# Performance work log

Measured on AMD Instinct MI355X. Metric: run time of the kernel, lower is better.

Reference implementation:

```python
import jax, jax.numpy as jnp
import numpy as np

# ---------- e3nn-style machinery, max_l = 1, real basis ----------
_EPS3 = np.zeros((3, 3, 3), dtype=np.float64)
_EPS3[0, 1, 2] = _EPS3[1, 2, 0] = _EPS3[2, 0, 1] = 1.0
_EPS3[0, 2, 1] = _EPS3[2, 1, 0] = _EPS3[1, 0, 2] = -1.0
W3J = {
    (0, 0, 0): np.ones((1, 1, 1)),
    (0, 1, 1): np.eye(3)[None, :, :] / np.sqrt(3.0),
    (1, 0, 1): np.eye(3)[:, None, :] / np.sqrt(3.0),
    (1, 1, 0): np.eye(3)[:, :, None] / np.sqrt(3.0),
    (1, 1, 1): _EPS3 / np.sqrt(6.0),
}

# irreps as (mul, l, parity)
IR_SH    = [(1, 0, 1), (1, 1, -1)]                      # 1x0e+1x1o (dim 4)
IR_INTER = [(4, 0, 1), (4, 0, -1), (2, 1, -1), (2, 1, 1)]  # gate.irreps_in (dim 20)
IR_GOUT  = [(2, 0, 1), (2, 0, -1), (2, 1, -1), (2, 1, 1)]  # gate.irreps_out (dim 16)
IR_OUT   = [(1, 1, -1), (1, 1, 1)]                      # 1x1o+1x1e (dim 6)

def _offsets(ir):
    off, o = [], 0
    for m, l, _ in ir:
        off.append(o)
        o += m * (2 * l + 1)
    return off, o

def build_tp(ir1, ir2, iro):
    """Fully-connected TP instructions: component irrep-norm, element path-norm."""
    fan = [0.0] * len(iro)
    paths = []
    for io, (mo, lo, po) in enumerate(iro):
        for i1, (m1, l1, p1) in enumerate(ir1):
            for i2, (m2, l2, p2) in enumerate(ir2):
                if p1 * p2 == po and abs(l1 - l2) <= lo <= l1 + l2:
                    paths.append((i1, i2, io))
                    fan[io] += m1 * m2
    ins, woff = [], 0
    for i1, i2, io in paths:
        m1, l1, _ = ir1[i1]; m2, l2, _ = ir2[i2]; mo, lo, _ = iro[io]
        alpha = float(np.sqrt((2 * lo + 1) / fan[io]))
        ins.append((i1, i2, io, alpha, woff))
        woff += m1 * m2 * mo
    return ins, woff

INS1, NUMEL1 = build_tp(IR_SH, IR_SH, IR_INTER)   # weight_numel = 14
INS2, NUMEL2 = build_tp(IR_GOUT, IR_SH, IR_OUT)   # weight_numel = 12

def tp_apply(ir1, ir2, iro, ins, x1, x2, w):
    off1, _ = _offsets(ir1); off2, _ = _offsets(ir2); offo, _ = _offsets(iro)
    lead = x1.shape[:-1]
    out = [None] * len(iro)
    for i1, i2, io, alpha, woff in ins:
        m1, l1, _ = ir1[i1]; m2, l2, _ = ir2[i2]; mo, lo, _ = iro[io]
        x1b = x1[..., off1[i1]:off1[i1] + m1 * (2 * l1 + 1)].reshape(lead + (m1, 2 * l1 + 1))
        x2b = x2[..., off2[i2]:off2[i2] + m2 * (2 * l2 + 1)].reshape(lead + (m2, 2 * l2 + 1))
        wb = w[..., woff:woff + m1 * m2 * mo].reshape(lead + (m1, m2, mo))
        C = jnp.asarray(W3J[(l1, l2, lo)], dtype=x1.dtype)
        blk = alpha * jnp.einsum('...ui,...vj,ijk,...uvw->...wk', x1b, x2b, C, wb)
        out[io] = blk if out[io] is None else out[io] + blk
    pieces = []
    for io, (mo, lo, _) in enumerate(iro):
        b = out[io] if out[io] is not None else jnp.zeros(lead + (mo, 2 * lo + 1), x1.dtype)
        pieces.append(b.reshape(lead + (mo * (2 * lo + 1),)))
    return jnp.concatenate(pieces, axis=-1)

def fc_net(x, w1, w2):
    # e3nn FullyConnectedNet: h = relu(x @ W1 / sqrt(fan_in)) * sqrt(2); out = h @ W2 / sqrt(fan)
    h = jax.nn.relu(x @ w1 / np.sqrt(w1.shape[0])) * np.sqrt(2.0)
    return h @ w2 / np.sqrt(w2.shape[0])

def gate_fn(x):
    # input irreps: [4x0e | 4x0o | 2x1o | 2x1e]; within 0e: 2 scalars + gates g1,g3; within 0o: 2 scalars + gates g2,g4
    lead = x.shape[:-1]
    se = jax.nn.relu(x[..., 0:2])
    ge = x[..., 2:4]
    so = jnp.abs(x[..., 4:6])
    go = x[..., 6:8]
    v1o = x[..., 8:14].reshape(lead + (2, 3))
    v1e = x[..., 14:20].reshape(lead + (2, 3))
    g1 = jax.nn.relu(ge[..., 0:1]); g3 = jax.nn.relu(ge[..., 1:2])
    g2 = jnp.tanh(go[..., 0:1]);    g4 = jnp.tanh(go[..., 1:2])
    v1o_out = jnp.concatenate([v1o[..., 0, :] * g1, v1o[..., 1, :] * g2], axis=-1)
    v1e_out = jnp.concatenate([v1e[..., 0, :] * g3, v1e[..., 1, :] * g4], axis=-1)
    return jnp.concatenate([se, so, v1o_out, v1e_out], axis=-1)  # [..., 16]

def sph_l1(d):
    # spherical harmonics l<=1, normalize=True, normalization='component' (e3nn l=1 order: y,z,x)
    n = jnp.sqrt(jnp.sum(d * d, axis=-1, keepdims=True) + 1e-12)
    u = d / n
    ones = jnp.ones(d.shape[:-1] + (1,), d.dtype)
    return jnp.concatenate([ones, np.sqrt(3.0) * u[..., [1, 2, 0]]], axis=-1)  # [..., 4]

def global_conv(ir1, iro, ins, nf, edge_attr, atten, normalizer, w1, w2):
    w = fc_net(atten, w1, w2)                                   # [B,N,N,numel]
    B, N = nf.shape[0], nf.shape[1]
    nfe = jnp.broadcast_to(nf[:, None, :, :], (B, N, N, nf.shape[-1]))  # node j at edge (i,j)
    ef = tp_apply(ir1, IR_SH, iro, ins, nfe, edge_attr, w)      # [B,N,N,dim_out]
    return jnp.sum(ef, axis=1) / normalizer

def _forward(attn_disp, attn_mask, coordinates, fc1_w1, fc1_w2, fc2_w1, fc2_w2):
    B, H, N, _ = attn_disp.shape
    normalizer = jnp.sqrt(jnp.sum((~jnp.isinf(attn_disp[:, 0])).astype(coordinates.dtype), axis=-1))[..., None]  # [B,N,1]
    ad = jnp.transpose(attn_disp, (0, 2, 3, 1))                 # [B,N,N,H]
    ad = jnp.where(jnp.isinf(ad), jnp.zeros((), ad.dtype), ad)
    # unit displacement (zero on diagonal)
    d = coordinates[:, :, None, :] - coordinates[:, None, :, :]
    d = d / (jnp.sqrt(jnp.sum(d * d, axis=-1, keepdims=True) + 1e-12) + 1e-5)
    edge_features = sph_l1(d)                                   # [B,N,N,4]
    nf = jnp.sum(edge_features, axis=1) / normalizer            # [B,N,4]
    nf = global_conv(IR_SH, IR_INTER, INS1, nf, edge_features, ad, normalizer, fc1_w1, fc1_w2)   # [B,N,20]
    nf = gate_fn(nf)                                            # [B,N,16]
    nf = global_conv(IR_GOUT, IR_OUT, INS2, nf, edge_features, ad, normalizer, fc2_w1, fc2_w2)   # [B,N,6]
    return ad, attn_mask, coordinates, nf, edge_features

def setup_inputs() -> dict:
    key = jax.random.key(0)
    ks = jax.random.split(key, 8)
    B, H, N = 4, 16, 512
    return {
        'attn_disp': jax.random.normal(ks[0], (B, H, N, N), jnp.float32),
        'attn_mask': jax.random.normal(ks[1], (B * H, N, N), jnp.float32),
        'coordinates': jax.random.normal(ks[2], (B, N, 3), jnp.float32),
        'fc1_w1': jax.random.normal(ks[3], (H, 2 * H), jnp.float32),
        'fc1_w2': jax.random.normal(ks[4], (2 * H, NUMEL1), jnp.float32),
        'fc2_w1': jax.random.normal(ks[5], (H, 2 * H), jnp.float32),
        'fc2_w2': jax.random.normal(ks[6], (2 * H, NUMEL2), jnp.float32),
    }

def reference(attn_disp, attn_mask, coordinates, fc1_w1, fc1_w2, fc2_w1, fc2_w2):
    return _forward(attn_disp, attn_mask, coordinates, fc1_w1, fc1_w2, fc2_w1, fc2_w2)
```

## Files before the change

kernel.cpp:

```cpp
#include <hip/hip_runtime.h>
#include <cmath>

#define NN 512

__device__ __forceinline__ int is_inf_f(float x) {
    return (__float_as_uint(x) & 0x7fffffffu) == 0x7f800000u;
}

__device__ __forceinline__ void edge_vec(float ci0, float ci1, float ci2,
                                         float cj0, float cj1, float cj2,
                                         float& e0, float& e1, float& e2) {
    float d0 = ci0 - cj0, d1 = ci1 - cj1, d2 = ci2 - cj2;
    float den = sqrtf(d0*d0 + d1*d1 + d2*d2 + 1e-12f) + 1e-5f;
    float r = 1.0f / den;
    d0 *= r; d1 *= r; d2 *= r;
    float n = sqrtf(d0*d0 + d1*d1 + d2*d2 + 1e-12f);
    float s = 1.7320508075688772f / n;
    e0 = d1 * s;
    e1 = d2 * s;
    e2 = d0 * s;
}

__global__ __launch_bounds__(256) void k_trans(
    const float* __restrict__ disp, const float* __restrict__ coords,
    float* __restrict__ ad_out, float* __restrict__ adT_out,
    float* __restrict__ ef_out, float* __restrict__ ws_norm)
{
    __shared__ float L[256 * 20];
    const int blk = blockIdx.x;
    const int b   = blk >> 7;
    const int i0  = (blk & 127) << 2;
    const int tid = threadIdx.x;
    const int il  = tid >> 6;
    const int jl  = tid & 63;
    const int i   = i0 + il;
    const float ci0 = coords[(b*NN+i)*3+0];
    const float ci1 = coords[(b*NN+i)*3+1];
    const float ci2 = coords[(b*NN+i)*3+2];
    int cnt = 0;
    for (int ch = 0; ch < 8; ch++) {
        const int j = ch*64 + jl;
        float v[16];
        #pragma unroll
        for (int h = 0; h < 16; h++) {
            float x = disp[(size_t)((b*16+h)*NN + i)*NN + j];
            int bad = is_inf_f(x);
            if (h == 0) cnt += 1 - bad;
            v[h] = bad ? 0.0f : x;
        }
        float4* dst = (float4*)(ad_out + (size_t)((b*NN+i)*NN + j)*16);
        dst[0] = make_float4(v[0], v[1], v[2], v[3]);
        dst[1] = make_float4(v[4], v[5], v[6], v[7]);
        dst[2] = make_float4(v[8], v[9], v[10], v[11]);
        dst[3] = make_float4(v[12], v[13], v[14], v[15]);
        {
            const float cj0 = coords[(b*NN+j)*3+0];
            const float cj1 = coords[(b*NN+j)*3+1];
            const float cj2 = coords[(b*NN+j)*3+2];
            float e0, e1, e2;
            edge_vec(ci0, ci1, ci2, cj0, cj1, cj2, e0, e1, e2);
            ((float4*)ef_out)[(size_t)(b*NN+i)*NN + j] = make_float4(1.0f, e0, e1, e2);
        }
        {
            float4* Lr = (float4*)(L + tid*20);
            Lr[0] = make_float4(v[0], v[1], v[2], v[3]);
            Lr[1] = make_float4(v[4], v[5], v[6], v[7]);
            Lr[2] = make_float4(v[8], v[9], v[10], v[11]);
            Lr[3] = make_float4(v[12], v[13], v[14], v[15]);
        }
        __syncthreads();
        #pragma unroll
        for (int p = 0; p < 4; p++) {
            const int jj  = (tid >> 4) + p*16;
            const int f   = tid & 15;
            const int iw  = f >> 2, w4 = f & 3;
            const int row = iw*64 + jj;
            float4 val = *(const float4*)(L + row*20 + w4*4);
            ((float4*)adT_out)[(size_t)((b*NN + ch*64 + jj)*NN + (i0 + iw))*4 + w4] = val;
        }
        __syncthreads();
    }
    #pragma unroll
    for (int off = 32; off >= 1; off >>= 1) cnt += __shfl_xor(cnt, off);
    if (jl == 0) ws_norm[b*NN + i] = sqrtf((float)cnt);
}

__global__ __launch_bounds__(256) void k_reduce2(
    const float* __restrict__ adT, const float* __restrict__ coords,
    const float* __restrict__ wA, const float* __restrict__ wB,
    float* __restrict__ ws)
{
    const int blk  = blockIdx.x;
    const int b    = blk >> 9, j = blk & 511;
    const int tid  = threadIdx.x;
    const int lane = tid & 63;
    const int wv   = tid >> 6;
    const float cj0 = coords[(b*NN+j)*3+0];
    const float cj1 = coords[(b*NN+j)*3+1];
    const float cj2 = coords[(b*NN+j)*3+2];
    float e0[8], e1[8], e2[8];
    float se0 = 0.f, se1 = 0.f, se2 = 0.f;
    #pragma unroll
    for (int k = 0; k < 8; k++) {
        const int i = k*64 + lane;
        const float ci0 = coords[(b*NN+i)*3+0];
        const float ci1 = coords[(b*NN+i)*3+1];
        const float ci2 = coords[(b*NN+i)*3+2];
        edge_vec(ci0, ci1, ci2, cj0, cj1, cj2, e0[k], e1[k], e2[k]);
        se0 += e0[k]; se1 += e1[k]; se2 += e2[k];
    }
    const float* __restrict__ W = (wv & 2) ? wB : wA;
    const int cbase = (wv & 1) * 16;
    const size_t abase = (size_t)((b*NN + j) * NN) * 16;
    float* accg = ws + 2048*4 + (size_t)blk*256;
    for (int cb = 0; cb < 4; cb++) {
        float wt[4][16];
        #pragma unroll
        for (int cc = 0; cc < 4; cc++) {
            const int col = __builtin_amdgcn_readfirstlane(cbase + cb*4 + cc);
            #pragma unroll
            for (int h = 0; h < 16; h++) wt[cc][h] = W[h*32 + col];
        }
        float acc[4][4];
        #pragma unroll
        for (int cc = 0; cc < 4; cc++)
            #pragma unroll
            for (int w = 0; w < 4; w++) acc[cc][w] = 0.f;
        float4 A0, A1, A2, A3;
        {
            const float4* s = (const float4*)(adT + abase + (size_t)lane*16);
            A0 = s[0]; A1 = s[1]; A2 = s[2]; A3 = s[3];
        }
        #pragma unroll
        for (int k = 0; k < 8; k++) {
            float4 N0, N1, N2, N3;
            if (k < 7) {
                const float4* s = (const float4*)(adT + abase + (size_t)((k+1)*64 + lane)*16);
                N0 = s[0]; N1 = s[1]; N2 = s[2]; N3 = s[3];
            }
            #pragma unroll
            for (int cc = 0; cc < 4; cc++) {
                float t;
                t = A0.x * wt[cc][0];
                t = fmaf(A0.y, wt[cc][1],  t);
                t = fmaf(A0.z, wt[cc][2],  t);
                t = fmaf(A0.w, wt[cc][3],  t);
                t = fmaf(A1.x, wt[cc][4],  t);
                t = fmaf(A1.y, wt[cc][5],  t);
                t = fmaf(A1.z, wt[cc][6],  t);
                t = fmaf(A1.w, wt[cc][7],  t);
                t = fmaf(A2.x, wt[cc][8],  t);
                t = fmaf(A2.y, wt[cc][9],  t);
                t = fmaf(A2.z, wt[cc][10], t);
                t = fmaf(A2.w, wt[cc][11], t);
                t = fmaf(A3.x, wt[cc][12], t);
                t = fmaf(A3.y, wt[cc][13], t);
                t = fmaf(A3.z, wt[cc][14], t);
                t = fmaf(A3.w, wt[cc][15], t);
                const float hq = fmaxf(t * 0.25f, 0.f) * 1.4142135623730951f;
                acc[cc][0] += hq;
                acc[cc][1] = fmaf(e0[k], hq, acc[cc][1]);
                acc[cc][2] = fmaf(e1[k], hq, acc[cc][2]);
                acc[cc][3] = fmaf(e2[k], hq, acc[cc][3]);
            }
            A0 = N0; A1 = N1; A2 = N2; A3 = N3;
        }
        #pragma unroll
        for (int cc = 0; cc < 4; cc++)
            #pragma unroll
            for (int w = 0; w < 4; w++) {
                float vs = acc[cc][w];
                vs += __shfl_xor(vs, 1);  vs += __shfl_xor(vs, 2);
                vs += __shfl_xor(vs, 4);  vs += __shfl_xor(vs, 8);
                vs += __shfl_xor(vs, 16); vs += __shfl_xor(vs, 32);
                const int q = cc*4 + w;
                if (lane == q) {
                    const int C = wv*16 + cb*4 + cc;
                    accg[((C >> 5)*4 + w)*32 + (C & 31)] = vs;
                }
            }
    }
    if (wv == 0) {
        #pragma unroll
        for (int off = 1; off < 64; off <<= 1) {
            se0 += __shfl_xor(se0, off);
            se1 += __shfl_xor(se1, off);
            se2 += __shfl_xor(se2, off);
        }
        if (lane == 0) {
            float* seg = ws + 2048 + blk*3;
            seg[0] = se0; seg[1] = se1; seg[2] = se2;
        }
    }
}

__global__ __launch_bounds__(256) void k_final(
    const float* __restrict__ ws,
    const float* __restrict__ w2a,
    const float* __restrict__ w2b,
    float* __restrict__ nf_out,
    const float* __restrict__ mask, float* __restrict__ mask_out,
    const float* __restrict__ coords, float* __restrict__ coords_out)
{
    if (blockIdx.x >= 8) {
        const int cblk = blockIdx.x - 8;
        const float4* mi = (const float4*)mask;
        float4* mo = (float4*)mask_out;
        const size_t base = (size_t)cblk * 8192;
        #pragma unroll
        for (int r = 0; r < 32; r++) mo[base + r*256 + threadIdx.x] = mi[base + r*256 + threadIdx.x];
        if (cblk == 0) {
            for (int idx = threadIdx.x; idx < 4*NN*3; idx += 256) coords_out[idx] = coords[idx];
        }
        return;
    }
    const int bj = blockIdx.x*256 + threadIdx.x;
    const float inv = 1.0f / ws[bj];
    const float s  = 512.0f * inv;
    const float vv0 = ws[2048 + bj*3 + 0] * inv;
    const float vv1 = ws[2048 + bj*3 + 1] * inv;
    const float vv2 = ws[2048 + bj*3 + 2] * inv;
    const float* acc = ws + 2048*4 + (size_t)bj*256;
    const float ksc = 0.17677669529663687f;
    float S0[14], S1[3][14];
    #pragma unroll
    for (int cc = 0; cc < 14; cc++) { S0[cc]=0.f; S1[0][cc]=0.f; S1[1][cc]=0.f; S1[2][cc]=0.f; }
    for (int c = 0; c < 32; c++) {
        const float p = acc[c], q0 = acc[32+c], q1 = acc[64+c], q2 = acc[96+c];
        #pragma unroll
        for (int cc = 0; cc < 14; cc++) {
            const float w = w2a[c*14+cc];
            S0[cc]    = fmaf(p,  w, S0[cc]);
            S1[0][cc] = fmaf(q0, w, S1[0][cc]);
            S1[1][cc] = fmaf(q1, w, S1[1][cc]);
            S1[2][cc] = fmaf(q2, w, S1[2][cc]);
        }
    }
    #pragma unroll
    for (int cc = 0; cc < 14; cc++) { S0[cc]*=ksc; S1[0][cc]*=ksc; S1[1][cc]*=ksc; S1[2][cc]*=ksc; }
    const float is2 = 0.7071067811865476f;
    const float is3 = 0.5773502691896258f;
    float x0[4];
    #pragma unroll
    for (int k = 0; k < 4; k++)
        x0[k] = inv*is2*( s*S0[k] + is3*(vv0*S1[0][4+k] + vv1*S1[1][4+k] + vv2*S1[2][4+k]) );
    const float vv[3] = {vv0, vv1, vv2};
    float x8[3];
    #pragma unroll
    for (int k = 0; k < 3; k++)
        x8[k] = inv*is2*( s*S1[k][8] + vv[k]*S0[10] );
    const float E12_0=S1[0][12], E12_1=S1[1][12], E12_2=S1[2][12];
    float x14[3];
    x14[0] = inv*is2*(vv1*E12_2 - vv2*E12_1);
    x14[1] = inv*is2*(vv2*E12_0 - vv0*E12_2);
    x14[2] = inv*is2*(vv0*E12_1 - vv1*E12_0);
    const float a0 = fmaxf(x0[0],0.f), a1 = fmaxf(x0[1],0.f);
    const float g1 = fmaxf(x0[2],0.f), g3 = fmaxf(x0[3],0.f);
    const float p0=x8[0]*g1,  p1=x8[1]*g1,  p2=x8[2]*g1;
    const float q0_=x14[0]*g3, q1_=x14[1]*g3, q2_=x14[2]*g3;
    float T0[12], T1[3][12];
    #pragma unroll
    for (int cc = 0; cc < 12; cc++){ T0[cc]=0.f; T1[0][cc]=0.f; T1[1][cc]=0.f; T1[2][cc]=0.f; }
    const float* acc2 = acc + 128;
    for (int c = 0; c < 32; c++) {
        const float p = acc2[c], r0 = acc2[32+c], r1 = acc2[64+c], r2 = acc2[96+c];
        #pragma unroll
        for (int cc = 0; cc < 12; cc++) {
            const float w = w2b[c*12+cc];
            T0[cc]    = fmaf(p,  w, T0[cc]);
            T1[0][cc] = fmaf(r0, w, T1[0][cc]);
            T1[1][cc] = fmaf(r1, w, T1[1][cc]);
            T1[2][cc] = fmaf(r2, w, T1[2][cc]);
        }
    }
    #pragma unroll
    for (int cc = 0; cc < 12; cc++){ T0[cc]*=ksc; T1[0][cc]*=ksc; T1[1][cc]*=ksc; T1[2][cc]*=ksc; }
    const float is6  = 0.4082482904638631f;
    const float is12 = 0.28867513459481287f;
    const float E0[3] = {T1[0][0], T1[1][0], T1[2][0]};
    const float E1[3] = {T1[0][1], T1[1][1], T1[2][1]};
    const float E4[3] = {T1[0][4], T1[1][4], T1[2][4]};
    const float E8[3] = {T1[0][8], T1[1][8], T1[2][8]};
    const float cq0 = q1_*E4[2] - q2_*E4[1];
    const float cq1 = q2_*E4[0] - q0_*E4[2];
    const float cq2 = q0_*E4[1] - q1_*E4[0];
    const float cp0 = p1*E8[2] - p2*E8[1];
    const float cp1 = p2*E8[0] - p0*E8[2];
    const float cp2 = p0*E8[1] - p1*E8[0];
    float o[6];
    o[0] = inv*( is6*(a0*E0[0] + a1*E1[0]) + is6*p0*T0[2] + is12*cq0 );
    o[1] = inv*( is6*(a0*E0[1] + a1*E1[1]) + is6*p1*T0[2] + is12*cq1 );
    o[2] = inv*( is6*(a0*E0[2] + a1*E1[2]) + is6*p2*T0[2] + is12*cq2 );
    o[3] = inv*( is12*cp0 + is6*q0_*T0[10] );
    o[4] = inv*( is12*cp1 + is6*q1_*T0[10] );
    o[5] = inv*( is12*cp2 + is6*q2_*T0[10] );
    #pragma unroll
    for (int k = 0; k < 6; k++) nf_out[bj*6+k] = o[k];
}

extern "C" void kernel_launch(void* const* d_in, const int* in_sizes, int n_in,
                              void* d_out, int out_size, void* d_ws, size_t ws_size,
                              hipStream_t stream) {
    const float* disp   = (const float*)d_in[0];
    const float* mask   = (const float*)d_in[1];
    const float* coords = (const float*)d_in[2];
    const float* fc1w1  = (const float*)d_in[3];
    const float* fc1w2  = (const float*)d_in[4];
    const float* fc2w1  = (const float*)d_in[5];
    const float* fc2w2  = (const float*)d_in[6];
    float* out = (float*)d_out;
    float* ad_out     = out;
    float* mask_out   = out + 16777216;
    float* coords_out = out + 33554432;
    float* nf_out     = coords_out + 6144;
    float* ef_out     = nf_out + 12288;
    float* ws = (float*)d_ws;

    float* adT = mask_out;

    k_trans  <<<512,  256, 0, stream>>>(disp, coords, ad_out, adT, ef_out, ws);
    k_reduce2<<<2048, 256, 0, stream>>>(adT, coords, fc1w1, fc2w1, ws);
    k_final  <<<520,  256, 0, stream>>>(ws, fc1w2, fc2w2, nf_out,
                                        mask, mask_out, coords, coords_out);
}
```

Before: 414.9 us.

## Restructure edge reduction so each lane owns one weight column across i-range

```diff
diff --git a/kernel.cpp b/kernel.cpp
--- a/kernel.cpp
+++ b/kernel.cpp
@@ -85,11 +85,14 @@
     if (jl == 0) ws_norm[b*NN + i] = sqrtf((float)cnt);
 }
 
-__global__ __launch_bounds__(256) void k_reduce2(
+__global__ __launch_bounds__(256) void k_reduce3(
     const float* __restrict__ adT, const float* __restrict__ coords,
     const float* __restrict__ wA, const float* __restrict__ wB,
     float* __restrict__ ws)
 {
+    __shared__ float4 E4[NN];
+    __shared__ float4 R4[4*64];
+    __shared__ float  sred[12];
     const int blk  = blockIdx.x;
     const int b    = blk >> 9, j = blk & 511;
     const int tid  = threadIdx.x;
@@ -98,99 +101,79 @@
     const float cj0 = coords[(b*NN+j)*3+0];
     const float cj1 = coords[(b*NN+j)*3+1];
     const float cj2 = coords[(b*NN+j)*3+2];
-    float e0[8], e1[8], e2[8];
     float se0 = 0.f, se1 = 0.f, se2 = 0.f;
     #pragma unroll
-    for (int k = 0; k < 8; k++) {
-        const int i = k*64 + lane;
+    for (int r = 0; r < 2; r++) {
+        const int i = r*256 + tid;
         const float ci0 = coords[(b*NN+i)*3+0];
         const float ci1 = coords[(b*NN+i)*3+1];
         const float ci2 = coords[(b*NN+i)*3+2];
-        edge_vec(ci0, ci1, ci2, cj0, cj1, cj2, e0[k], e1[k], e2[k]);
-        se0 += e0[k]; se1 += e1[k]; se2 += e2[k];
-    }
-    const float* __restrict__ W = (wv & 2) ? wB : wA;
-    const int cbase = (wv & 1) * 16;
-    const size_t abase = (size_t)((b*NN + j) * NN) * 16;
-    float* accg = ws + 2048*4 + (size_t)blk*256;
-    for (int cb = 0; cb < 4; cb++) {
-        float wt[4][16];
-        #pragma unroll
-        for (int cc = 0; cc < 4; cc++) {
-            const int col = __builtin_amdgcn_readfirstlane(cbase + cb*4 + cc);
-            #pragma unroll
-            for (int h = 0; h < 16; h++) wt[cc][h] = W[h*32 + col];
-        }
-        float acc[4][4];
-        #pragma unroll
-        for (int cc = 0; cc < 4; cc++)
-            #pragma unroll
-            for (int w = 0; w < 4; w++) acc[cc][w] = 0.f;
-        float4 A0, A1, A2, A3;
-        {
-            const float4* s = (const float4*)(adT + abase + (size_t)lane*16);
-            A0 = s[0]; A1 = s[1]; A2 = s[2]; A3 = s[3];
-        }
-        #pragma unroll
-        for (int k = 0; k < 8; k++) {
-            float4 N0, N1, N2, N3;
-            if (k < 7) {
-                const float4* s = (const float4*)(adT + abase + (size_t)((k+1)*64 + lane)*16);
-                N0 = s[0]; N1 = s[1]; N2 = s[2]; N3 = s[3];
-            }
-            #pragma unroll
-            for (int cc = 0; cc < 4; cc++) {
-                float t;
-                t = A0.x * wt[cc][0];
-                t = fmaf(A0.y, wt[cc][1],  t);
-                t = fmaf(A0.z, wt[cc][2],  t);
-                t = fmaf(A0.w, wt[cc][3],  t);
-                t = fmaf(A1.x, wt[cc][4],  t);
-                t = fmaf(A1.y, wt[cc][5],  t);
-                t = fmaf(A1.z, wt[cc][6],  t);
-                t = fmaf(A1.w, wt[cc][7],  t);
-                t = fmaf(A2.x, wt[cc][8],  t);
-                t = fmaf(A2.y, wt[cc][9],  t);
-                t = fmaf(A2.z, wt[cc][10], t);
-                t = fmaf(A2.w, wt[cc][11], t);
-                t = fmaf(A3.x, wt[cc][12], t);
-                t = fmaf(A3.y, wt[cc][13], t);
-                t = fmaf(A3.z, wt[cc][14], t);
-                t = fmaf(A3.w, wt[cc][15], t);
-                const float hq = fmaxf(t * 0.25f, 0.f) * 1.4142135623730951f;
-                acc[cc][0] += hq;
-                acc[cc][1] = fmaf(e0[k], hq, acc[cc][1]);
-                acc[cc][2] = fmaf(e1[k], hq, acc[cc][2]);
-                acc[cc][3] = fmaf(e2[k], hq, acc[cc][3]);
-            }
-            A0 = N0; A1 = N1; A2 = N2; A3 = N3;
-        }
-        #pragma unroll
-        for (int cc = 0; cc < 4; cc++)
-            #pragma unroll
-            for (int w = 0; w < 4; w++) {
-                float vs = acc[cc][w];
-                vs += __shfl_xor(vs, 1);  vs += __shfl_xor(vs, 2);
-                vs += __shfl_xor(vs, 4);  vs += __shfl_xor(vs, 8);
-                vs += __shfl_xor(vs, 16); vs += __shfl_xor(vs, 32);
-                const int q = cc*4 + w;
-                if (lane == q) {
-                    const int C = wv*16 + cb*4 + cc;
-                    accg[((C >> 5)*4 + w)*32 + (C & 31)] = vs;
-                }
-            }
-    }
-    if (wv == 0) {
-        #pragma unroll
-        for (int off = 1; off < 64; off <<= 1) {
-            se0 += __shfl_xor(se0, off);
-            se1 += __shfl_xor(se1, off);
-            se2 += __shfl_xor(se2, off);
-        }
-        if (lane == 0) {
-            float* seg = ws + 2048 + blk*3;
-            seg[0] = se0; seg[1] = se1; seg[2] = se2;
-        }
+        float e0, e1, e2;
+        edge_vec(ci0, ci1, ci2, cj0, cj1, cj2, e0, e1, e2);
+        E4[i] = make_float4(e0, e1, e2, 0.f);
+        se0 += e0; se1 += e1; se2 += e2;
+    }
+    const float* __restrict__ Wsel = (lane < 32) ? wA : wB;
+    const int cl = lane & 31;
+    float w[16];
+    #pragma unroll
+    for (int h = 0; h < 16; h++) w[h] = Wsel[h*32 + cl];
+    __syncthreads();
+    const float* __restrict__ Arow = adT + (size_t)((b*NN + j) * NN) * 16;
+    float acc0 = 0.f, acc1 = 0.f, acc2 = 0.f, acc3 = 0.f;
+    const int ibase = wv * 128;
+    #pragma unroll 4
+    for (int k = 0; k < 128; k++) {
+        const int i = ibase + k;
+        const float4* Ap = (const float4*)(Arow + (size_t)i * 16);
+        const float4 a0 = Ap[0], a1 = Ap[1], a2 = Ap[2], a3 = Ap[3];
+        const float4 ev = E4[i];
+        float t;
+        t = a0.x * w[0];
+        t = fmaf(a0.y, w[1],  t);
+        t = fmaf(a0.z, w[2],  t);
+        t = fmaf(a0.w, w[3],  t);
+        t = fmaf(a1.x, w[4],  t);
+        t = fmaf(a1.y, w[5],  t);
+        t = fmaf(a1.z, w[6],  t);
+        t = fmaf(a1.w, w[7],  t);
+        t = fmaf(a2.x, w[8],  t);
+        t = fmaf(a2.y, w[9],  t);
+        t = fmaf(a2.z, w[10], t);
+        t = fmaf(a2.w, w[11], t);
+        t = fmaf(a3.x, w[12], t);
+        t = fmaf(a3.y, w[13], t);
+        t = fmaf(a3.z, w[14], t);
+        t = fmaf(a3.w, w[15], t);
+        const float m = fmaxf(t, 0.f);
+        acc0 += m;
+        acc1 = fmaf(ev.x, m, acc1);
+        acc2 = fmaf(ev.y, m, acc2);
+        acc3 = fmaf(ev.z, m, acc3);
+    }
+    R4[wv*64 + lane] = make_float4(acc0, acc1, acc2, acc3);
+    #pragma unroll
+    for (int off = 1; off < 64; off <<= 1) {
+        se0 += __shfl_xor(se0, off);
+        se1 += __shfl_xor(se1, off);
+        se2 += __shfl_xor(se2, off);
+    }
+    if (lane == 0) { sred[wv*3+0] = se0; sred[wv*3+1] = se1; sred[wv*3+2] = se2; }
+    __syncthreads();
+    {
+        const int col = tid & 63, wq = tid >> 6;
+        const float* Rf = (const float*)R4;
+        float v = Rf[(0*64+col)*4 + wq] + Rf[(1*64+col)*4 + wq]
+                + Rf[(2*64+col)*4 + wq] + Rf[(3*64+col)*4 + wq];
+        v *= 0.35355339059327373f;
+        float* accg = ws + 2048*4 + (size_t)blk*256;
+        accg[((col >> 5)*4 + wq)*32 + (col & 31)] = v;
+    }
+    if (tid == 0) {
+        float* seg = ws + 2048 + blk*3;
+        seg[0] = sred[0]+sred[3]+sred[6]+sred[9];
+        seg[1] = sred[1]+sred[4]+sred[7]+sred[10];
+        seg[2] = sred[2]+sred[5]+sred[8]+sred[11];
     }
 }
 
@@ -319,7 +302,7 @@
     float* adT = mask_out;
 
     k_trans  <<<512,  256, 0, stream>>>(disp, coords, ad_out, adT, ef_out, ws);
-    k_reduce2<<<2048, 256, 0, stream>>>(adT, coords, fc1w1, fc2w1, ws);
+    k_reduce3<<<2048, 256, 0, stream>>>(adT, coords, fc1w1, fc2w1, ws);
     k_final  <<<520,  256, 0, stream>>>(ws, fc1w2, fc2w2, nf_out,
                                         mask, mask_out, coords, coords_out);
 }
```

Result: slower. 436.8 us (+5.3%).
